# Kernel tuning notes

Hardware: AMD Instinct MI355X
Metric: run time of the kernel (lower is better)

The kernel has to match this reference:

```python
import jax, jax.numpy as jnp
import numpy as np

B, S, E, H = 2, 2048, 768, 12
HD = E // H
EPS = 1e-5


def setup_inputs() -> dict:
    key = jax.random.key(0)
    ks = jax.random.split(key, 7)
    sc_in = 1.0 / np.sqrt(E)
    return {
        "x": jax.random.normal(ks[0], (B, S, E), dtype=jnp.float32),
        "gamma": jnp.ones((E,), dtype=jnp.float32),
        "beta": jnp.zeros((E,), dtype=jnp.float32),
        "Wqkv": jax.random.normal(ks[1], (3 * E, E), dtype=jnp.float32) * sc_in,
        "bqkv": jax.random.normal(ks[2], (3 * E,), dtype=jnp.float32) * 0.01,
        "Wo": jax.random.normal(ks[3], (E, E), dtype=jnp.float32) * sc_in,
        "bo": jax.random.normal(ks[4], (E,), dtype=jnp.float32) * 0.01,
    }


def reference(x, gamma, beta, Wqkv, bqkv, Wo, bo):
    # LayerNorm
    mu = jnp.mean(x, axis=-1, keepdims=True)
    var = jnp.mean(jnp.square(x - mu), axis=-1, keepdims=True)
    xn = (x - mu) * jax.lax.rsqrt(var + EPS) * gamma + beta
    # fused QKV projection; original reshapes to [B,S,H,3*hd] then chunks,
    # i.e. per-head blocks of 3*hd split into q/k/v slices of hd each.
    qkv = (xn @ Wqkv.T + bqkv).reshape(B, S, H, 3, HD)
    q, k, v = qkv[..., 0, :], qkv[..., 1, :], qkv[..., 2, :]  # [B,S,H,hd]
    scores = jnp.einsum("bshd,bthd->bhst", q, k) / np.sqrt(HD)
    attn = jax.nn.softmax(scores, axis=-1)  # [B,H,S,S]
    out = jnp.einsum("bhst,bthd->bshd", attn, v).reshape(B, S, E)
    return out @ Wo.T + bo
```

## Files before the change

kernel.cpp:

```cpp
#include <hip/hip_runtime.h>
#include <math.h>

#define B_  2
#define S_  2048
#define E_  768
#define H_  12
#define HD_ 64
#define M_  (B_ * S_)
#define N3E (3 * E_)

typedef __attribute__((ext_vector_type(8)))  short short8;
typedef __attribute__((ext_vector_type(4)))  float floatx4;
typedef __attribute__((ext_vector_type(16))) float floatx16;

#define QSCALE 0.18033688011112042f

__device__ inline unsigned short f2bf(float f) {
  union { float f; unsigned u; } a; a.f = f;
  unsigned r = a.u + 0x7fff + ((a.u >> 16) & 1);
  return (unsigned short)(r >> 16);
}
__device__ inline unsigned short f2bf_fast(float f) {
  union { float f; unsigned u; } a; a.f = f;
  return (unsigned short)((a.u + 0x8000u) >> 16);
}

__global__ __launch_bounds__(256) void cvt_kernel(
    const float* __restrict__ src, unsigned short* __restrict__ dst, int n4) {
  int i = blockIdx.x * 256 + threadIdx.x;
  if (i < n4) {
    float4 f = *(const float4*)&src[i * 4];
    ushort4 r;
    r.x = f2bf(f.x); r.y = f2bf(f.y); r.z = f2bf(f.z); r.w = f2bf(f.w);
    *(ushort4*)&dst[i * 4] = r;
  }
}

__global__ __launch_bounds__(256) void ln_kernel(
    const float* __restrict__ x, const float* __restrict__ gamma,
    const float* __restrict__ beta, unsigned short* __restrict__ xnb) {
  const int row = blockIdx.x;
  const int t = threadIdx.x;
  const float* xr = x + (size_t)row * E_;

  float v0 = xr[t];
  float v1 = xr[t + 256];
  float v2 = xr[t + 512];
  float s  = v0 + v1 + v2;
  float s2 = v0 * v0 + v1 * v1 + v2 * v2;

  for (int o = 32; o > 0; o >>= 1) {
    s  += __shfl_down(s, o);
    s2 += __shfl_down(s2, o);
  }
  __shared__ float red[8];
  const int wave = t >> 6, lane = t & 63;
  if (lane == 0) { red[wave] = s; red[4 + wave] = s2; }
  __syncthreads();
  s  = red[0] + red[1] + red[2] + red[3];
  s2 = red[4] + red[5] + red[6] + red[7];

  const float mu  = s * (1.0f / E_);
  const float var = s2 * (1.0f / E_) - mu * mu;
  const float rs  = rsqrtf(var + 1e-5f);

  unsigned short* xo = xnb + (size_t)row * E_;
  xo[t]       = f2bf((v0 - mu) * rs * gamma[t]       + beta[t]);
  xo[t + 256] = f2bf((v1 - mu) * rs * gamma[t + 256] + beta[t + 256]);
  xo[t + 512] = f2bf((v2 - mu) * rs * gamma[t + 512] + beta[t + 512]);
}

__global__ __launch_bounds__(256) void bgemm_kernel(
    const unsigned short* __restrict__ A, const unsigned short* __restrict__ Wb,
    const float* __restrict__ bias, int mode,
    unsigned short* __restrict__ qbf, unsigned short* __restrict__ kbf,
    unsigned short* __restrict__ vtb, float* __restrict__ out) {
  __shared__ __align__(16) unsigned short As[128 * 64];
  __shared__ __align__(16) unsigned short Bs[128 * 64];

  const int t  = threadIdx.x;
  const int ln = t & 63, wv = t >> 6;
  const int lr = ln & 15, lg = ln >> 4;
  const int wr = wv >> 1, wc = wv & 1;
  const int m0 = blockIdx.x * 128, n0 = blockIdx.y * 128;

  const int srow = ln >> 3;
  const int scol = (ln & 7) * 8;

  const unsigned short* Ag = A  + (size_t)(m0 + wv * 32 + srow) * 768 + scol;
  const unsigned short* Bg = Wb + (size_t)(n0 + wv * 32 + srow) * 768 + scol;

  floatx4 acc[4][4];
#pragma unroll
  for (int i = 0; i < 4; i++)
#pragma unroll
    for (int j = 0; j < 4; j++) acc[i][j] = (floatx4){0.f, 0.f, 0.f, 0.f};

  for (int k0 = 0; k0 < 768; k0 += 64) {
    __syncthreads();
#pragma unroll
    for (int j = 0; j < 4; j++) {
      __builtin_amdgcn_global_load_lds(
          (const __attribute__((address_space(1))) void*)(Ag + k0 + j * 8 * 768),
          (__attribute__((address_space(3))) void*)(&As[(wv * 32 + j * 8) * 64]),
          16, 0, 0);
      __builtin_amdgcn_global_load_lds(
          (const __attribute__((address_space(1))) void*)(Bg + k0 + j * 8 * 768),
          (__attribute__((address_space(3))) void*)(&Bs[(wv * 32 + j * 8) * 64]),
          16, 0, 0);
    }
    __syncthreads();

#pragma unroll
    for (int kk = 0; kk < 2; kk++) {
      short8 af[4], bf[4];
#pragma unroll
      for (int i = 0; i < 4; i++)
        af[i] = *(const short8*)&As[(wr * 64 + i * 16 + lr) * 64 + kk * 32 + lg * 8];
#pragma unroll
      for (int j = 0; j < 4; j++)
        bf[j] = *(const short8*)&Bs[(wc * 64 + j * 16 + lr) * 64 + kk * 32 + lg * 8];
#pragma unroll
      for (int i = 0; i < 4; i++)
#pragma unroll
        for (int j = 0; j < 4; j++)
          acc[i][j] = __builtin_amdgcn_mfma_f32_16x16x32_bf16(af[i], bf[j], acc[i][j], 0, 0, 0);
    }
  }

  if (mode == 1) {
#pragma unroll
    for (int i = 0; i < 4; i++) {
      const int grow0 = m0 + wr * 64 + i * 16 + lg * 4;
#pragma unroll
      for (int j = 0; j < 4; j++) {
        const int gcol = n0 + wc * 64 + j * 16 + lr;
        const float bb = bias[gcol];
#pragma unroll
        for (int r = 0; r < 4; r++)
          out[(size_t)(grow0 + r) * E_ + gcol] = acc[i][j][r] + bb;
      }
    }
  } else {
#pragma unroll
    for (int i = 0; i < 4; i++) {
      const int grow0 = m0 + wr * 64 + i * 16 + lg * 4;
      const int bq = grow0 >> 11, s0 = grow0 & 2047;
      const int tb = s0 >> 6, kh = (s0 >> 5) & 1;
#pragma unroll
      for (int j = 0; j < 4; j++) {
        const int n = n0 + wc * 64 + j * 16 + lr;
        const int h = n / 192, w = (n >> 6) % 3, d = n & 63;
        const int bh = bq * H_ + h;
        const float bb = bias[n];
        if (w == 2) {
          const int db = d >> 5, l31v = d & 31;
          const int kc2 = (s0 >> 4) & 1, l5v = (s0 >> 3) & 1, e0 = s0 & 7;
          ushort4 rv;
          rv.x = f2bf(acc[i][j][0] + bb);
          rv.y = f2bf(acc[i][j][1] + bb);
          rv.z = f2bf(acc[i][j][2] + bb);
          rv.w = f2bf(acc[i][j][3] + bb);
          const size_t idx =
              ((((((size_t)bh * 32 + tb) * 2 + kh) * 2 + db) * 2 + kc2) * 2 + l5v) * 256
              + (size_t)l31v * 8 + e0;
          *(ushort4*)&vtb[idx] = rv;
        } else {
          unsigned short* dst = (w == 0) ? qbf : kbf;
          const float sc = (w == 0) ? QSCALE : 1.0f;
          const int kc = d >> 4, l5 = (d >> 3) & 1, e = d & 7;
          const size_t basei =
              ((((size_t)bh * 32 + tb) * 2 + kh) * 4 + kc) * 512 + (size_t)l5 * 256 + e;
          const int r0 = (s0 & 31) * 8;
#pragma unroll
          for (int r = 0; r < 4; r++)
            dst[basei + r0 + r * 8] = f2bf((acc[i][j][r] + bb) * sc);
        }
      }
    }
  }
}

#define PROW 40

__global__ __launch_bounds__(256, 3) void attn_kernel(
    const unsigned short* __restrict__ qb, const unsigned short* __restrict__ kb,
    const unsigned short* __restrict__ vtb, unsigned short* __restrict__ ao) {
  __shared__ __align__(16) unsigned short Ps[4 * 32 * PROW];
  __shared__ __align__(16) float Cmb[2 * 64 * 36];

  const int t = threadIdx.x;
  const int lane = t & 63, wv = t >> 6;
  const int l31 = lane & 31, l5 = lane >> 5;
  const int wq = wv & 1, kh = wv >> 1;

  const int id = blockIdx.x;
  const int bh = (id & 7) * 3 + ((id >> 3) >> 5);
  const int qt = (id >> 3) & 31;
  const int b = bh / H_, h = bh % H_;
  const int q0 = qt * 64;

  short8 qf[4];
  {
    const unsigned short* qp =
        qb + ((((size_t)bh * 32 + qt) * 2 + wq) * 4) * 512 + (size_t)lane * 8;
#pragma unroll
    for (int kc = 0; kc < 4; kc++) qf[kc] = *(const short8*)(qp + kc * 512);
  }
  short8 ones;
#pragma unroll
  for (int i = 0; i < 8; i++) ones[i] = (short)0x3F80;

  floatx16 oacc0 = (floatx16)0.0f;
  floatx16 oacc1 = (floatx16)0.0f;
  floatx16 lacc  = (floatx16)0.0f;

  const unsigned short* kpb = kb  + ((size_t)bh * 64 + kh) * 2048 + (size_t)lane * 8;
  const unsigned short* vpb = vtb + ((size_t)bh * 64 + kh) * 2048 + (size_t)lane * 8;
  unsigned short* PsW = &Ps[wv * 32 * PROW];

  short8 kf[4];
#pragma unroll
  for (int kc = 0; kc < 4; kc++) kf[kc] = *(const short8*)(kpb + kc * 512);

  for (int tb = 0; tb < 32; tb++) {
    const unsigned short* vt = vpb + (size_t)tb * 4096;
    short8 vf0 = *(const short8*)(vt);
    short8 vf1 = *(const short8*)(vt + 512);
    short8 vf2 = *(const short8*)(vt + 1024);
    short8 vf3 = *(const short8*)(vt + 1536);

    floatx16 sacc = (floatx16)0.0f;
#pragma unroll
    for (int kc = 0; kc < 4; kc++)
      sacc = __builtin_amdgcn_mfma_f32_32x32x16_bf16(kf[kc], qf[kc], sacc, 0, 0, 0);

    {
      const unsigned short* kt = kpb + (size_t)((tb + 1) & 31) * 4096;
#pragma unroll
      for (int kc = 0; kc < 4; kc++) kf[kc] = *(const short8*)(kt + kc * 512);
    }

#pragma unroll
    for (int r = 0; r < 16; r++) sacc[r] = exp2f(sacc[r]);
#pragma unroll
    for (int rq = 0; rq < 4; rq++) {
      ushort4 w;
      w.x = f2bf_fast(sacc[rq * 4 + 0]);
      w.y = f2bf_fast(sacc[rq * 4 + 1]);
      w.z = f2bf_fast(sacc[rq * 4 + 2]);
      w.w = f2bf_fast(sacc[rq * 4 + 3]);
      *(ushort4*)&PsW[l31 * PROW + rq * 8 + l5 * 4] = w;
    }

    const unsigned short* prd = &PsW[l31 * PROW + l5 * 8];
    short8 pf0 = *(const short8*)(prd);
    short8 pf1 = *(const short8*)(prd + 16);

    oacc0 = __builtin_amdgcn_mfma_f32_32x32x16_bf16(vf0, pf0, oacc0, 0, 0, 0);
    oacc0 = __builtin_amdgcn_mfma_f32_32x32x16_bf16(vf1, pf1, oacc0, 0, 0, 0);
    oacc1 = __builtin_amdgcn_mfma_f32_32x32x16_bf16(vf2, pf0, oacc1, 0, 0, 0);
    oacc1 = __builtin_amdgcn_mfma_f32_32x32x16_bf16(vf3, pf1, oacc1, 0, 0, 0);
    lacc  = __builtin_amdgcn_mfma_f32_32x32x16_bf16(ones, pf0, lacc, 0, 0, 0);
    lacc  = __builtin_amdgcn_mfma_f32_32x32x16_bf16(ones, pf1, lacc, 0, 0, 0);
  }

  float* cw = &Cmb[(size_t)(wq * 64 + lane) * 36];
  if (kh == 1) {
#pragma unroll
    for (int rq = 0; rq < 4; rq++) {
      float4 w0, w1;
      w0.x = oacc0[rq * 4 + 0]; w0.y = oacc0[rq * 4 + 1];
      w0.z = oacc0[rq * 4 + 2]; w0.w = oacc0[rq * 4 + 3];
      w1.x = oacc1[rq * 4 + 0]; w1.y = oacc1[rq * 4 + 1];
      w1.z = oacc1[rq * 4 + 2]; w1.w = oacc1[rq * 4 + 3];
      *(float4*)&cw[rq * 4]      = w0;
      *(float4*)&cw[16 + rq * 4] = w1;
    }
    cw[32] = lacc[0];
  }
  __syncthreads();
  if (kh == 0) {
    const float inv = 1.0f / (lacc[0] + cw[32]);
    const int row = q0 + wq * 32 + l31;
    unsigned short* arow = &ao[((size_t)(b * S_ + row)) * E_ + h * HD_];
#pragma unroll
    for (int rq = 0; rq < 4; rq++) {
      ushort4 s0, s1;
      s0.x = f2bf((oacc0[rq * 4 + 0] + cw[rq * 4 + 0]) * inv);
      s0.y = f2bf((oacc0[rq * 4 + 1] + cw[rq * 4 + 1]) * inv);
      s0.z = f2bf((oacc0[rq * 4 + 2] + cw[rq * 4 + 2]) * inv);
      s0.w = f2bf((oacc0[rq * 4 + 3] + cw[rq * 4 + 3]) * inv);
      s1.x = f2bf((oacc1[rq * 4 + 0] + cw[16 + rq * 4 + 0]) * inv);
      s1.y = f2bf((oacc1[rq * 4 + 1] + cw[16 + rq * 4 + 1]) * inv);
      s1.z = f2bf((oacc1[rq * 4 + 2] + cw[16 + rq * 4 + 2]) * inv);
      s1.w = f2bf((oacc1[rq * 4 + 3] + cw[16 + rq * 4 + 3]) * inv);
      *(ushort4*)&arow[8 * rq + 4 * l5]      = s0;
      *(ushort4*)&arow[32 + 8 * rq + 4 * l5] = s1;
    }
  }
}

extern "C" void kernel_launch(void* const* d_in, const int* in_sizes, int n_in,
                              void* d_out, int out_size, void* d_ws, size_t ws_size,
                              hipStream_t stream) {
  const float* x     = (const float*)d_in[0];
  const float* gamma = (const float*)d_in[1];
  const float* beta  = (const float*)d_in[2];
  const float* Wqkv  = (const float*)d_in[3];
  const float* bqkv  = (const float*)d_in[4];
  const float* Wo    = (const float*)d_in[5];
  const float* bo    = (const float*)d_in[6];
  float* out = (float*)d_out;

  const size_t SZ = (size_t)M_ * E_;
  unsigned short* xnb = (unsigned short*)d_ws;
  unsigned short* qbf = xnb + SZ;
  unsigned short* kbf = qbf + SZ;
  unsigned short* vtb = kbf + SZ;
  unsigned short* aob = vtb + SZ;
  unsigned short* wqb = aob + SZ;
  unsigned short* wob = wqb + (size_t)N3E * E_;

  const int nq4 = (N3E * E_) / 4;
  const int no4 = (E_ * E_) / 4;
  cvt_kernel<<<(nq4 + 255) / 256, 256, 0, stream>>>(Wqkv, wqb, nq4);
  cvt_kernel<<<(no4 + 255) / 256, 256, 0, stream>>>(Wo, wob, no4);

  ln_kernel<<<M_, 256, 0, stream>>>(x, gamma, beta, xnb);

  dim3 g_qkv(M_ / 128, N3E / 128);
  bgemm_kernel<<<g_qkv, 256, 0, stream>>>(xnb, wqb, bqkv, 0, qbf, kbf, vtb, nullptr);

  attn_kernel<<<768, 256, 0, stream>>>(qbf, kbf, vtb, aob);

  dim3 g_out(M_ / 128, E_ / 128);
  bgemm_kernel<<<g_out, 256, 0, stream>>>(aob, wob, bo, 1, nullptr, nullptr, nullptr, out);
}
```

Baseline: 188.4 us.

## Split attention keys four ways per block and store V and P in fp16

The attention kernel now gives each block 32 query rows instead of 64, with all four waves splitting the key range four ways. The grid doubles to 1536 blocks, occupancy is raised to 4 blocks per CU, and the partial outputs and row sums are combined through shared memory in a two-stage reduction. V and the softmax probabilities switch from bf16 to fp16 (packed round-toward-zero converts and f16 MFMA), and Q/K stores use the cheaper rounding. This trades extra reduction traffic and a second barrier for more parallelism and cheaper conversions, with some precision risk if unnormalized exp values overflow fp16.

Measured after the change: 193.1 us. +2.5%, slower.

```diff
diff --git a/kernel.cpp b/kernel.cpp
--- a/kernel.cpp
+++ b/kernel.cpp
@@ -10,6 +10,9 @@
 #define N3E (3 * E_)
 
 typedef __attribute__((ext_vector_type(8)))  short short8;
+typedef __attribute__((ext_vector_type(8)))  _Float16 half8;
+typedef __attribute__((ext_vector_type(4)))  _Float16 half4;
+typedef __attribute__((ext_vector_type(2)))  _Float16 half2_t;
 typedef __attribute__((ext_vector_type(4)))  float floatx4;
 typedef __attribute__((ext_vector_type(16))) float floatx16;
 
@@ -23,6 +26,9 @@
 __device__ inline unsigned short f2bf_fast(float f) {
   union { float f; unsigned u; } a; a.f = f;
   return (unsigned short)((a.u + 0x8000u) >> 16);
+}
+__device__ inline half2_t pkrtz(float a, float b) {
+  return __builtin_bit_cast(half2_t, __builtin_amdgcn_cvt_pkrtz(a, b));
 }
 
 __global__ __launch_bounds__(256) void cvt_kernel(
@@ -74,7 +80,7 @@
     const unsigned short* __restrict__ A, const unsigned short* __restrict__ Wb,
     const float* __restrict__ bias, int mode,
     unsigned short* __restrict__ qbf, unsigned short* __restrict__ kbf,
-    unsigned short* __restrict__ vtb, float* __restrict__ out) {
+    _Float16* __restrict__ vth, float* __restrict__ out) {
   __shared__ __align__(16) unsigned short As[128 * 64];
   __shared__ __align__(16) unsigned short Bs[128 * 64];
 
@@ -156,15 +162,13 @@
         if (w == 2) {
           const int db = d >> 5, l31v = d & 31;
           const int kc2 = (s0 >> 4) & 1, l5v = (s0 >> 3) & 1, e0 = s0 & 7;
-          ushort4 rv;
-          rv.x = f2bf(acc[i][j][0] + bb);
-          rv.y = f2bf(acc[i][j][1] + bb);
-          rv.z = f2bf(acc[i][j][2] + bb);
-          rv.w = f2bf(acc[i][j][3] + bb);
+          half2_t h01 = pkrtz(acc[i][j][0] + bb, acc[i][j][1] + bb);
+          half2_t h23 = pkrtz(acc[i][j][2] + bb, acc[i][j][3] + bb);
+          half4 hv = __builtin_shufflevector(h01, h23, 0, 1, 2, 3);
           const size_t idx =
               ((((((size_t)bh * 32 + tb) * 2 + kh) * 2 + db) * 2 + kc2) * 2 + l5v) * 256
               + (size_t)l31v * 8 + e0;
-          *(ushort4*)&vtb[idx] = rv;
+          *(half4*)&vth[idx] = hv;
         } else {
           unsigned short* dst = (w == 0) ? qbf : kbf;
           const float sc = (w == 0) ? QSCALE : 1.0f;
@@ -174,7 +178,7 @@
           const int r0 = (s0 & 31) * 8;
 #pragma unroll
           for (int r = 0; r < 4; r++)
-            dst[basei + r0 + r * 8] = f2bf((acc[i][j][r] + bb) * sc);
+            dst[basei + r0 + r * 8] = f2bf_fast((acc[i][j][r] + bb) * sc);
         }
       }
     }
@@ -183,52 +187,55 @@
 
 #define PROW 40
 
-__global__ __launch_bounds__(256, 3) void attn_kernel(
+__global__ __launch_bounds__(256, 4) void attn_kernel(
     const unsigned short* __restrict__ qb, const unsigned short* __restrict__ kb,
-    const unsigned short* __restrict__ vtb, unsigned short* __restrict__ ao) {
-  __shared__ __align__(16) unsigned short Ps[4 * 32 * PROW];
-  __shared__ __align__(16) float Cmb[2 * 64 * 36];
+    const _Float16* __restrict__ vth, unsigned short* __restrict__ ao) {
+  __shared__ __align__(16) unsigned char smem[26112];
+  _Float16* Ps = (_Float16*)smem;
+  float* C1 = (float*)smem;
+  float* C2 = C1 + 3 * 64 * 17;
 
   const int t = threadIdx.x;
   const int lane = t & 63, wv = t >> 6;
   const int l31 = lane & 31, l5 = lane >> 5;
-  const int wq = wv & 1, kh = wv >> 1;
 
   const int id = blockIdx.x;
-  const int bh = (id & 7) * 3 + ((id >> 3) >> 5);
-  const int qt = (id >> 3) & 31;
+  const int bh = (id & 7) * 3 + ((id >> 3) >> 6);
+  const int qt = (id >> 3) & 63;
   const int b = bh / H_, h = bh % H_;
-  const int q0 = qt * 64;
+  const int q0 = qt * 32;
 
   short8 qf[4];
   {
     const unsigned short* qp =
-        qb + ((((size_t)bh * 32 + qt) * 2 + wq) * 4) * 512 + (size_t)lane * 8;
+        qb + ((size_t)(bh * 32 + (qt >> 1)) * 2 + (qt & 1)) * 2048 + (size_t)lane * 8;
 #pragma unroll
     for (int kc = 0; kc < 4; kc++) qf[kc] = *(const short8*)(qp + kc * 512);
   }
-  short8 ones;
-#pragma unroll
-  for (int i = 0; i < 8; i++) ones[i] = (short)0x3F80;
+  half8 ones;
+#pragma unroll
+  for (int i = 0; i < 8; i++) ones[i] = (_Float16)1.0f;
 
   floatx16 oacc0 = (floatx16)0.0f;
   floatx16 oacc1 = (floatx16)0.0f;
   floatx16 lacc  = (floatx16)0.0f;
 
-  const unsigned short* kpb = kb  + ((size_t)bh * 64 + kh) * 2048 + (size_t)lane * 8;
-  const unsigned short* vpb = vtb + ((size_t)bh * 64 + kh) * 2048 + (size_t)lane * 8;
-  unsigned short* PsW = &Ps[wv * 32 * PROW];
+  const unsigned short* kpb =
+      kb + (size_t)(bh * 32 + (wv >> 1)) * 4096 + (size_t)(wv & 1) * 2048 + (size_t)lane * 8;
+  const _Float16* vpb =
+      vth + (size_t)(bh * 32 + (wv >> 1)) * 4096 + (size_t)(wv & 1) * 2048 + (size_t)lane * 8;
+  _Float16* PsW = Ps + wv * 32 * PROW;
 
   short8 kf[4];
 #pragma unroll
   for (int kc = 0; kc < 4; kc++) kf[kc] = *(const short8*)(kpb + kc * 512);
 
-  for (int tb = 0; tb < 32; tb++) {
-    const unsigned short* vt = vpb + (size_t)tb * 4096;
-    short8 vf0 = *(const short8*)(vt);
-    short8 vf1 = *(const short8*)(vt + 512);
-    short8 vf2 = *(const short8*)(vt + 1024);
-    short8 vf3 = *(const short8*)(vt + 1536);
+  for (int tb = 0; tb < 16; tb++) {
+    const _Float16* vt = vpb + (size_t)tb * 8192;
+    half8 vf0 = *(const half8*)(vt);
+    half8 vf1 = *(const half8*)(vt + 512);
+    half8 vf2 = *(const half8*)(vt + 1024);
+    half8 vf3 = *(const half8*)(vt + 1536);
 
     floatx16 sacc = (floatx16)0.0f;
 #pragma unroll
@@ -236,7 +243,7 @@
       sacc = __builtin_amdgcn_mfma_f32_32x32x16_bf16(kf[kc], qf[kc], sacc, 0, 0, 0);
 
     {
-      const unsigned short* kt = kpb + (size_t)((tb + 1) & 31) * 4096;
+      const unsigned short* kt = kpb + (size_t)((tb + 1) & 15) * 8192;
 #pragma unroll
       for (int kc = 0; kc < 4; kc++) kf[kc] = *(const short8*)(kt + kc * 512);
     }
@@ -245,58 +252,77 @@
     for (int r = 0; r < 16; r++) sacc[r] = exp2f(sacc[r]);
 #pragma unroll
     for (int rq = 0; rq < 4; rq++) {
-      ushort4 w;
-      w.x = f2bf_fast(sacc[rq * 4 + 0]);
-      w.y = f2bf_fast(sacc[rq * 4 + 1]);
-      w.z = f2bf_fast(sacc[rq * 4 + 2]);
-      w.w = f2bf_fast(sacc[rq * 4 + 3]);
-      *(ushort4*)&PsW[l31 * PROW + rq * 8 + l5 * 4] = w;
-    }
-
-    const unsigned short* prd = &PsW[l31 * PROW + l5 * 8];
-    short8 pf0 = *(const short8*)(prd);
-    short8 pf1 = *(const short8*)(prd + 16);
-
-    oacc0 = __builtin_amdgcn_mfma_f32_32x32x16_bf16(vf0, pf0, oacc0, 0, 0, 0);
-    oacc0 = __builtin_amdgcn_mfma_f32_32x32x16_bf16(vf1, pf1, oacc0, 0, 0, 0);
-    oacc1 = __builtin_amdgcn_mfma_f32_32x32x16_bf16(vf2, pf0, oacc1, 0, 0, 0);
-    oacc1 = __builtin_amdgcn_mfma_f32_32x32x16_bf16(vf3, pf1, oacc1, 0, 0, 0);
-    lacc  = __builtin_amdgcn_mfma_f32_32x32x16_bf16(ones, pf0, lacc, 0, 0, 0);
-    lacc  = __builtin_amdgcn_mfma_f32_32x32x16_bf16(ones, pf1, lacc, 0, 0, 0);
-  }
-
-  float* cw = &Cmb[(size_t)(wq * 64 + lane) * 36];
-  if (kh == 1) {
-#pragma unroll
-    for (int rq = 0; rq < 4; rq++) {
-      float4 w0, w1;
-      w0.x = oacc0[rq * 4 + 0]; w0.y = oacc0[rq * 4 + 1];
-      w0.z = oacc0[rq * 4 + 2]; w0.w = oacc0[rq * 4 + 3];
-      w1.x = oacc1[rq * 4 + 0]; w1.y = oacc1[rq * 4 + 1];
-      w1.z = oacc1[rq * 4 + 2]; w1.w = oacc1[rq * 4 + 3];
-      *(float4*)&cw[rq * 4]      = w0;
-      *(float4*)&cw[16 + rq * 4] = w1;
-    }
-    cw[32] = lacc[0];
-  }
+      half2_t a = pkrtz(sacc[rq * 4 + 0], sacc[rq * 4 + 1]);
+      half2_t c = pkrtz(sacc[rq * 4 + 2], sacc[rq * 4 + 3]);
+      half4 w = __builtin_shufflevector(a, c, 0, 1, 2, 3);
+      *(half4*)&PsW[l31 * PROW + rq * 8 + l5 * 4] = w;
+    }
+
+    const _Float16* prd = &PsW[l31 * PROW + l5 * 8];
+    half8 pf0 = *(const half8*)(prd);
+    half8 pf1 = *(const half8*)(prd + 16);
+
+    oacc0 = __builtin_amdgcn_mfma_f32_32x32x16_f16(vf0, pf0, oacc0, 0, 0, 0);
+    oacc0 = __builtin_amdgcn_mfma_f32_32x32x16_f16(vf1, pf1, oacc0, 0, 0, 0);
+    oacc1 = __builtin_amdgcn_mfma_f32_32x32x16_f16(vf2, pf0, oacc1, 0, 0, 0);
+    oacc1 = __builtin_amdgcn_mfma_f32_32x32x16_f16(vf3, pf1, oacc1, 0, 0, 0);
+    lacc  = __builtin_amdgcn_mfma_f32_32x32x16_f16(ones, pf0, lacc, 0, 0, 0);
+    lacc  = __builtin_amdgcn_mfma_f32_32x32x16_f16(ones, pf1, lacc, 0, 0, 0);
+  }
+
   __syncthreads();
-  if (kh == 0) {
-    const float inv = 1.0f / (lacc[0] + cw[32]);
-    const int row = q0 + wq * 32 + l31;
-    unsigned short* arow = &ao[((size_t)(b * S_ + row)) * E_ + h * HD_];
-#pragma unroll
-    for (int rq = 0; rq < 4; rq++) {
-      ushort4 s0, s1;
-      s0.x = f2bf((oacc0[rq * 4 + 0] + cw[rq * 4 + 0]) * inv);
-      s0.y = f2bf((oacc0[rq * 4 + 1] + cw[rq * 4 + 1]) * inv);
-      s0.z = f2bf((oacc0[rq * 4 + 2] + cw[rq * 4 + 2]) * inv);
-      s0.w = f2bf((oacc0[rq * 4 + 3] + cw[rq * 4 + 3]) * inv);
-      s1.x = f2bf((oacc1[rq * 4 + 0] + cw[16 + rq * 4 + 0]) * inv);
-      s1.y = f2bf((oacc1[rq * 4 + 1] + cw[16 + rq * 4 + 1]) * inv);
-      s1.z = f2bf((oacc1[rq * 4 + 2] + cw[16 + rq * 4 + 2]) * inv);
-      s1.w = f2bf((oacc1[rq * 4 + 3] + cw[16 + rq * 4 + 3]) * inv);
-      *(ushort4*)&arow[8 * rq + 4 * l5]      = s0;
-      *(ushort4*)&arow[32 + 8 * rq + 4 * l5] = s1;
+  if (wv > 0) {
+    float* c = &C1[(size_t)((wv - 1) * 64 + lane) * 17];
+#pragma unroll
+    for (int j = 0; j < 16; j++) c[j] = oacc0[j];
+    c[16] = lacc[0];
+  }
+  if (wv != 1) {
+    const int slot = (wv == 0) ? 0 : wv - 1;
+    float* c = &C2[(size_t)(slot * 64 + lane) * 17];
+#pragma unroll
+    for (int j = 0; j < 16; j++) c[j] = oacc1[j];
+    c[16] = lacc[0];
+  }
+  __syncthreads();
+  if (wv < 2) {
+    float o[16];
+    float L;
+    if (wv == 0) {
+      L = lacc[0];
+#pragma unroll
+      for (int j = 0; j < 16; j++) o[j] = oacc0[j];
+#pragma unroll
+      for (int i = 0; i < 3; i++) {
+        const float* c = &C1[(size_t)(i * 64 + lane) * 17];
+#pragma unroll
+        for (int j = 0; j < 16; j++) o[j] += c[j];
+        L += c[16];
+      }
+    } else {
+      L = lacc[0];
+#pragma unroll
+      for (int j = 0; j < 16; j++) o[j] = oacc1[j];
+#pragma unroll
+      for (int i = 0; i < 3; i++) {
+        const float* c = &C2[(size_t)(i * 64 + lane) * 17];
+#pragma unroll
+        for (int j = 0; j < 16; j++) o[j] += c[j];
+        L += c[16];
+      }
+    }
+    const float inv = 1.0f / L;
+    const int row = q0 + l31;
+    const int dbase = wv * 32;
+    unsigned short* arow = &ao[((size_t)(b * S_ + row)) * E_ + h * HD_ + dbase];
+#pragma unroll
+    for (int a = 0; a < 4; a++) {
+      ushort4 s;
+      s.x = f2bf(o[a * 4 + 0] * inv);
+      s.y = f2bf(o[a * 4 + 1] * inv);
+      s.z = f2bf(o[a * 4 + 2] * inv);
+      s.w = f2bf(o[a * 4 + 3] * inv);
+      *(ushort4*)&arow[8 * a + 4 * l5] = s;
     }
   }
 }
@@ -317,8 +343,8 @@
   unsigned short* xnb = (unsigned short*)d_ws;
   unsigned short* qbf = xnb + SZ;
   unsigned short* kbf = qbf + SZ;
-  unsigned short* vtb = kbf + SZ;
-  unsigned short* aob = vtb + SZ;
+  _Float16*       vth = (_Float16*)(kbf + SZ);
+  unsigned short* aob = (unsigned short*)(vth + SZ);
   unsigned short* wqb = aob + SZ;
   unsigned short* wob = wqb + (size_t)N3E * E_;
 
@@ -330,9 +356,9 @@
   ln_kernel<<<M_, 256, 0, stream>>>(x, gamma, beta, xnb);
 
   dim3 g_qkv(M_ / 128, N3E / 128);
-  bgemm_kernel<<<g_qkv, 256, 0, stream>>>(xnb, wqb, bqkv, 0, qbf, kbf, vtb, nullptr);
-
-  attn_kernel<<<768, 256, 0, stream>>>(qbf, kbf, vtb, aob);
+  bgemm_kernel<<<g_qkv, 256, 0, stream>>>(xnb, wqb, bqkv, 0, qbf, kbf, vth, nullptr);
+
+  attn_kernel<<<1536, 256, 0, stream>>>(qbf, kbf, vth, aob);
 
   dim3 g_out(M_ / 128, E_ / 128);
   bgemm_kernel<<<g_out, 256, 0, stream>>>(aob, wob, bo, 1, nullptr, nullptr, nullptr, out);
```
